# Optimization experiments

Hardware: AMD Instinct MI355X
Metric: run time of the kernel (lower is better)

The kernel has to match this reference:

```python
import jax, jax.numpy as jnp
import numpy as np

N, E, M, C = 4000, 60000, 16, 64        # nodes, edges, (lmax+1)^2, sphere_channels
H, HEADS, A, VC, CE, Z = 64, 8, 8, 8, 32, 90  # attn hidden, heads, alpha ch, value ch, edge ch, max elements


def _params(key):
    ks = jax.random.split(key, 10)
    g = lambda k, sh, fan: jax.random.normal(k, sh, dtype=jnp.float32) / np.float32(np.sqrt(fan))
    return [g(ks[0], (Z, CE), CE),          # emb_s: source atom embedding
            g(ks[1], (Z, CE), CE),          # emb_t: target atom embedding
            g(ks[2], (CE,), 1.0),           # w_d : distance projection
            g(ks[3], (CE, H), CE),          # We  : edge scalar -> hidden (m=0 inject)
            g(ks[4], (C, H), C),            # Ws  : source channel mix
            g(ks[5], (C, H), C),            # Wt  : target channel mix
            g(ks[6], (H, HEADS * A), H),    # Wa  : alpha features
            g(ks[7], (HEADS, A), A),        # va  : per-head alpha vector
            g(ks[8], (H, HEADS * VC), H),   # Wv  : values
            g(ks[9], (HEADS * VC, 1), HEADS * VC)]  # Wo : output proj (1 channel)


def setup_inputs() -> dict:
    key = jax.random.key(0)
    ks = jax.random.split(key, 8)
    x = jax.random.normal(ks[0], (N, M, C), dtype=jnp.float32)
    atomic_numbers = jax.random.randint(ks[1], (N,), 0, Z)
    edge_distance = jax.random.uniform(ks[2], (E,), dtype=jnp.float32) * 5.0 + 0.5
    edge_index = jax.random.randint(ks[3], (2, E), 0, N)
    noise_mask = jax.random.randint(ks[4], (N,), 0, 2).astype(bool)
    # per-edge SO3/Wigner rotation: random orthogonal [E, M, M]
    rng = np.random.default_rng(0)
    q, _ = np.linalg.qr(rng.standard_normal((E, M, M)).astype(np.float32))
    wigner = jnp.asarray(q, dtype=jnp.float32)
    names = ['emb_s', 'emb_t', 'w_d', 'We', 'Ws', 'Wt', 'Wa', 'va', 'Wv', 'Wo']
    inp = {'x': x, 'atomic_numbers': atomic_numbers, 'edge_distance': edge_distance,
           'edge_index': edge_index, 'noise_mask': noise_mask, 'wigner': wigner}
    for n, v in zip(names, _params(ks[5])):
        inp['fs_' + n] = v
    for n, v in zip(names, _params(ks[6])):
        inp['dn_' + n] = v
    return inp


def _block(x, zn, dist, src, dst, D, emb_s, emb_t, w_d, We, Ws, Wt, Wa, va, Wv, Wo):
    # gather + rotate edge-wise node features into edge-aligned frame
    xs = jnp.einsum('emn,enc->emc', D, x[src])            # [E,M,C]
    xt = jnp.einsum('emn,enc->emc', D, x[dst])            # [E,M,C]
    # scalar edge embedding (distance + source/target atom embeddings)
    e = jax.nn.silu(dist[:, None] * w_d + emb_s[zn[src]] + emb_t[zn[dst]])  # [E,CE]
    # SO2-style channel mixing; inject edge scalars into the m=0 (invariant) row
    f = jnp.einsum('emc,ch->emh', xs, Ws) + jnp.einsum('emc,ch->emh', xt, Wt)  # [E,M,H]
    f = f.at[:, 0, :].add(e @ We)
    # attention logits from the invariant part
    a = jax.nn.leaky_relu(f[:, 0, :] @ Wa, 0.2).reshape(E, HEADS, A)
    logits = jnp.einsum('eha,ha->eh', a, va)              # [E,HEADS]
    # segment softmax over incoming edges per target node
    mx = jax.ops.segment_max(logits, dst, num_segments=N)
    ex = jnp.exp(logits - mx[dst])
    alpha = ex / (jax.ops.segment_sum(ex, dst, num_segments=N)[dst] + 1e-9)
    # values, attention-weight, rotate back (D^T), scatter to nodes
    v = (f @ Wv).reshape(E, M, HEADS, VC) * alpha[:, None, :, None]
    v = jnp.einsum('emn,emhv->enhv', D, v).reshape(E, M, HEADS * VC)
    out = jax.ops.segment_sum(v, dst, num_segments=N) @ Wo  # [N,M,1]
    return out[:, 1:4, 0]  # narrow(1, 1, 3) -> l=1 vector components [N,3]


def reference(x, atomic_numbers, edge_distance, edge_index, noise_mask, wigner,
              fs_emb_s, fs_emb_t, fs_w_d, fs_We, fs_Ws, fs_Wt, fs_Wa, fs_va, fs_Wv, fs_Wo,
              dn_emb_s, dn_emb_t, dn_w_d, dn_We, dn_Ws, dn_Wt, dn_Wa, dn_va, dn_Wv, dn_Wo):
    src, dst = edge_index[0], edge_index[1]
    forces = _block(x, atomic_numbers, edge_distance, src, dst, wigner,
                    fs_emb_s, fs_emb_t, fs_w_d, fs_We, fs_Ws, fs_Wt, fs_Wa, fs_va, fs_Wv, fs_Wo)
    den = _block(x, atomic_numbers, edge_distance, src, dst, wigner,
                 dn_emb_s, dn_emb_t, dn_w_d, dn_We, dn_Ws, dn_Wt, dn_Wa, dn_va, dn_Wv, dn_Wo)
    # denoising_pos_forward with noise_mask: forces = den*mask + forces*~mask
    m = noise_mask[:, None].astype(x.dtype)
    return den * m + forces * (1.0 - m)
```

## Files before the change

kernel.cpp:

```cpp
#include <hip/hip_runtime.h>

typedef unsigned short ushort_t;
typedef __attribute__((ext_vector_type(8))) short short8;
typedef __attribute__((ext_vector_type(4))) float floatx4;

constexpr int RS = 11520;

__device__ inline float bf2f(ushort_t u) {
    union { unsigned int i; float f; } v; v.i = ((unsigned int)u) << 16; return v.f;
}
__device__ inline ushort_t f2bf(float f) {
    union { float f; unsigned int i; } v; v.f = f;
    unsigned int b = v.i + 0x7FFFu + ((v.i >> 16) & 1u);
    return (ushort_t)(b >> 16);
}

__global__ __launch_bounds__(256) void k_composites(
    const float* __restrict__ Ws0, const float* __restrict__ Wt0, const float* __restrict__ We0,
    const float* __restrict__ Wa0, const float* __restrict__ Wv0, const float* __restrict__ Wo0,
    const float* __restrict__ Ws1, const float* __restrict__ Wt1, const float* __restrict__ We1,
    const float* __restrict__ Wa1, const float* __restrict__ Wv1, const float* __restrict__ Wo1,
    float* __restrict__ cmp)
{
    int task = blockIdx.x;
    int r    = blockIdx.y;
    const float* Ws = r ? Ws1 : Ws0;
    const float* Wt = r ? Wt1 : Wt0;
    const float* We = r ? We1 : We0;
    const float* Wa = r ? Wa1 : Wa0;
    const float* Wv = r ? Wv1 : Wv0;
    const float* Wo = r ? Wo1 : Wo0;
    float* base = cmp + r * RS;

    if (task == 0 || task == 1) {
        const float* L = task ? Wt : Ws;
        float* out = base + task * 4096;
        for (int idx = threadIdx.x; idx < 4096; idx += 256) {
            int c = idx >> 6, j = idx & 63;
            float a = 0.f;
            for (int k = 0; k < 64; ++k) a += L[c * 64 + k] * Wa[k * 64 + j];
            out[idx] = a;
        }
    } else if (task == 2) {
        float* out = base + 8192;
        for (int idx = threadIdx.x; idx < 2048; idx += 256) {
            int ce = idx >> 6, j = idx & 63;
            float a = 0.f;
            for (int k = 0; k < 64; ++k) a += We[ce * 64 + k] * Wa[k * 64 + j];
            out[idx] = a;
        }
    } else {
        const float* L = (task == 3) ? Ws : (task == 4) ? Wt : We;
        int rows = (task == 5) ? 32 : 64;
        float* out = base + ((task == 3) ? 10240 : (task == 4) ? 10752 : 11264);
        for (int idx = threadIdx.x; idx < rows * 8; idx += 256) {
            int c = idx >> 3, h = idx & 7;
            float a = 0.f;
            for (int k = 0; k < 64; ++k) {
                float wv = 0.f;
                #pragma unroll
                for (int aa = 0; aa < 8; ++aa) wv += Wv[k * 64 + h * 8 + aa] * Wo[h * 8 + aa];
                a += L[c * 64 + k] * wv;
            }
            out[idx] = a;
        }
    }
}

__device__ inline short8 bfragW(const float* __restrict__ W, int colBase, int kBase,
                                int q, int n) {
    short8 f;
    #pragma unroll
    for (int j = 0; j < 8; ++j)
        f[j] = (short)f2bf(W[(kBase + q * 8 + j) * 64 + colBase + n]);
    return f;
}
__device__ inline short8 bfragP(const float* __restrict__ P0, const float* __restrict__ P1,
                                int kBase, int q, int n) {
    const float* P = (n < 8) ? P0 : P1;
    int c = n & 7;
    short8 f;
    #pragma unroll
    for (int j = 0; j < 8; ++j)
        f[j] = (short)f2bf(P[(kBase + q * 8 + j) * 8 + c]);
    return f;
}

#define MFMA(a, b, c) __builtin_amdgcn_mfma_f32_16x16x32_bf16((a), (b), (c), 0, 0, 0)

__global__ __launch_bounds__(256, 2) void k_node(
    const float* __restrict__ x, const int* __restrict__ mask,
    const float* __restrict__ cmp,
    float* __restrict__ psrc, float* __restrict__ ptgt,
    ushort_t* __restrict__ srcA, ushort_t* __restrict__ tgtA,
    int N, int totWaves)
{
    int wid  = (int)((blockIdx.x * blockDim.x + threadIdx.x) >> 6);
    int lane = threadIdx.x & 63;
    int q    = lane >> 4;
    int n16  = lane & 15;

    short8 Bs0[4][2], Bs1[4][2], Bt0[4][2], Bt1[4][2];
    #pragma unroll
    for (int t = 0; t < 4; ++t) {
        #pragma unroll
        for (int kh = 0; kh < 2; ++kh) {
            Bs0[t][kh] = bfragW(cmp,             t * 16, kh * 32, q, n16);
            Bs1[t][kh] = bfragW(cmp + RS,        t * 16, kh * 32, q, n16);
            Bt0[t][kh] = bfragW(cmp + 4096,      t * 16, kh * 32, q, n16);
            Bt1[t][kh] = bfragW(cmp + RS + 4096, t * 16, kh * 32, q, n16);
        }
    }
    short8 Bp[2], Bq[2];
    #pragma unroll
    for (int kh = 0; kh < 2; ++kh) {
        Bp[kh] = bfragP(cmp + 10240, cmp + RS + 10240, kh * 32, q, n16);
        Bq[kh] = bfragP(cmp + 10752, cmp + RS + 10752, kh * 32, q, n16);
    }

    const floatx4 zero = {0.f, 0.f, 0.f, 0.f};

    for (int nd = wid; nd < N; nd += totWaves) {
        const float* xp = x + (size_t)nd * 1024 + n16 * 64 + q * 8;
        float4 v0 = *(const float4*)(xp);
        float4 v1 = *(const float4*)(xp + 4);
        float4 v2 = *(const float4*)(xp + 32);
        float4 v3 = *(const float4*)(xp + 36);
        short8 a0, a1;
        a0[0] = (short)f2bf(v0.x); a0[1] = (short)f2bf(v0.y);
        a0[2] = (short)f2bf(v0.z); a0[3] = (short)f2bf(v0.w);
        a0[4] = (short)f2bf(v1.x); a0[5] = (short)f2bf(v1.y);
        a0[6] = (short)f2bf(v1.z); a0[7] = (short)f2bf(v1.w);
        a1[0] = (short)f2bf(v2.x); a1[1] = (short)f2bf(v2.y);
        a1[2] = (short)f2bf(v2.z); a1[3] = (short)f2bf(v2.w);
        a1[4] = (short)f2bf(v3.x); a1[5] = (short)f2bf(v3.y);
        a1[6] = (short)f2bf(v3.z); a1[7] = (short)f2bf(v3.w);

        int rsel = (mask[nd] != 0);

        {
            floatx4 c0 = zero, c1 = zero, c2 = zero, c3 = zero;
            c0 = MFMA(a0, Bs0[0][0], c0); c0 = MFMA(a1, Bs0[0][1], c0);
            c1 = MFMA(a0, Bs0[1][0], c1); c1 = MFMA(a1, Bs0[1][1], c1);
            c2 = MFMA(a0, Bs0[2][0], c2); c2 = MFMA(a1, Bs0[2][1], c2);
            c3 = MFMA(a0, Bs0[3][0], c3); c3 = MFMA(a1, Bs0[3][1], c3);
            ushort_t* sp = srcA + (size_t)nd * 2048 + (q * 4) * 64 + n16;
            #pragma unroll
            for (int rr = 0; rr < 4; ++rr) {
                sp[rr * 64 +  0] = f2bf(c0[rr]);
                sp[rr * 64 + 16] = f2bf(c1[rr]);
                sp[rr * 64 + 32] = f2bf(c2[rr]);
                sp[rr * 64 + 48] = f2bf(c3[rr]);
            }
        }
        {
            floatx4 c0 = zero, c1 = zero, c2 = zero, c3 = zero;
            c0 = MFMA(a0, Bs1[0][0], c0); c0 = MFMA(a1, Bs1[0][1], c0);
            c1 = MFMA(a0, Bs1[1][0], c1); c1 = MFMA(a1, Bs1[1][1], c1);
            c2 = MFMA(a0, Bs1[2][0], c2); c2 = MFMA(a1, Bs1[2][1], c2);
            c3 = MFMA(a0, Bs1[3][0], c3); c3 = MFMA(a1, Bs1[3][1], c3);
            ushort_t* sp = srcA + (size_t)nd * 2048 + 1024 + (q * 4) * 64 + n16;
            #pragma unroll
            for (int rr = 0; rr < 4; ++rr) {
                sp[rr * 64 +  0] = f2bf(c0[rr]);
                sp[rr * 64 + 16] = f2bf(c1[rr]);
                sp[rr * 64 + 32] = f2bf(c2[rr]);
                sp[rr * 64 + 48] = f2bf(c3[rr]);
            }
        }

        {
            floatx4 c0 = zero, c1 = zero, c2 = zero, c3 = zero;
            if (rsel) {
                c0 = MFMA(a0, Bt1[0][0], c0); c0 = MFMA(a1, Bt1[0][1], c0);
                c1 = MFMA(a0, Bt1[1][0], c1); c1 = MFMA(a1, Bt1[1][1], c1);
                c2 = MFMA(a0, Bt1[2][0], c2); c2 = MFMA(a1, Bt1[2][1], c2);
                c3 = MFMA(a0, Bt1[3][0], c3); c3 = MFMA(a1, Bt1[3][1], c3);
            } else {
                c0 = MFMA(a0, Bt0[0][0], c0); c0 = MFMA(a1, Bt0[0][1], c0);
                c1 = MFMA(a0, Bt0[1][0], c1); c1 = MFMA(a1, Bt0[1][1], c1);
                c2 = MFMA(a0, Bt0[2][0], c2); c2 = MFMA(a1, Bt0[2][1], c2);
                c3 = MFMA(a0, Bt0[3][0], c3); c3 = MFMA(a1, Bt0[3][1], c3);
            }
            ushort_t* tp = tgtA + (size_t)nd * 1024 + (q * 4) * 64 + n16;
            #pragma unroll
            for (int rr = 0; rr < 4; ++rr) {
                tp[rr * 64 +  0] = f2bf(c0[rr]);
                tp[rr * 64 + 16] = f2bf(c1[rr]);
                tp[rr * 64 + 32] = f2bf(c2[rr]);
                tp[rr * 64 + 48] = f2bf(c3[rr]);
            }
        }

        {
            floatx4 cp = zero;
            cp = MFMA(a0, Bp[0], cp); cp = MFMA(a1, Bp[1], cp);
            if (q == 0) {
                int r = n16 >> 3, h = n16 & 7;
                float* pp = psrc + (size_t)nd * 48 + r * 24 + h;
                pp[0]  = cp[1];
                pp[8]  = cp[2];
                pp[16] = cp[3];
            }
            floatx4 cq = zero;
            cq = MFMA(a0, Bq[0], cq); cq = MFMA(a1, Bq[1], cq);
            if (q == 0 && (n16 >> 3) == rsel) {
                int h = n16 & 7;
                float* pp = ptgt + (size_t)nd * 24 + h;
                pp[0]  = cq[1];
                pp[8]  = cq[2];
                pp[16] = cq[3];
            }
        }
    }
}

__global__ __launch_bounds__(256) void k_logits(
    const int* __restrict__ ei, const float* __restrict__ dist,
    const int* __restrict__ zn, const int* __restrict__ mask,
    const float* __restrict__ wig, const float* __restrict__ cmp,
    const float* __restrict__ embs0, const float* __restrict__ embt0, const float* __restrict__ wd0,
    const float* __restrict__ embs1, const float* __restrict__ embt1, const float* __restrict__ wd1,
    const float* __restrict__ va0, const float* __restrict__ va1,
    const ushort_t* __restrict__ srcA, const ushort_t* __restrict__ tgtA,
    float* __restrict__ den, float* __restrict__ exb, float* __restrict__ ejb, int E)
{
    int wv = threadIdx.x >> 6, j = threadIdx.x & 63;
    int e = blockIdx.x * 4 + wv;
    if (e >= E) return;
    int src = ei[e], dst = ei[E + e];
    int r = (mask[dst] != 0);
    float d = dist[e];
    int zs = zn[src], zt = zn[dst];

    float es;
    {
        int ce = j & 31;
        float z = r ? (d * wd1[ce] + embs1[zs * 32 + ce] + embt1[zt * 32 + ce])
                    : (d * wd0[ce] + embs0[zs * 32 + ce] + embt0[zt * 32 + ce]);
        es = z / (1.f + __expf(-z));
    }

    const float* WeWa   = cmp + r * RS + 8192;
    const float* WeWvWo = cmp + r * RS + 11264;
    int h8 = j & 7;
    float f0a = 0.f, ej = 0.f;
    #pragma unroll
    for (int ce = 0; ce < 32; ++ce) {
        float ev = __shfl(es, ce, 64);
        f0a += ev * WeWa[ce * 64 + j];
        ej  += ev * WeWvWo[ce * 8 + h8];
    }

    const ushort_t* sp = srcA + (size_t)src * 2048 + r * 1024 + j;
    const ushort_t* tp = tgtA + (size_t)dst * 1024 + j;
    const float* w0 = wig + (size_t)e * 256;
    #pragma unroll
    for (int n = 0; n < 16; ++n) {
        float sv = bf2f(sp[n * 64]) + bf2f(tp[n * 64]);
        f0a += w0[n] * sv;
    }

    float la = f0a > 0.f ? f0a : 0.2f * f0a;
    float val = la * (r ? va1[j] : va0[j]);
    val += __shfl_xor(val, 1);
    val += __shfl_xor(val, 2);
    val += __shfl_xor(val, 4);
    float ex = __expf(val);
    if (h8 == 0) {
        atomicAdd(&den[dst * 8 + (j >> 3)], ex);
        exb[(size_t)e * 8 + (j >> 3)] = ex;
    }
    if (j < 8) ejb[(size_t)e * 8 + j] = ej;
}

__global__ __launch_bounds__(256) void k_scatter(
    const int* __restrict__ ei, const int* __restrict__ mask,
    const float* __restrict__ wig,
    const float* __restrict__ psrc, const float* __restrict__ ptgt,
    const float* __restrict__ exb, const float* __restrict__ ejb,
    const float* __restrict__ den, float* __restrict__ out, int E)
{
    int t = threadIdx.x;
    int g = t >> 3, h = t & 7;
    int e = blockIdx.x * 32 + g;
    if (e >= E) return;
    int src = ei[e], dst = ei[E + e];
    int r = (mask[dst] != 0);
    float alpha = exb[(size_t)e * 8 + h] / (den[dst * 8 + h] + 1e-9f);
    const float* ps = psrc + (size_t)src * 48 + r * 24;
    const float* pt = ptgt + (size_t)dst * 24;
    float s0 = alpha * (ps[h]      + pt[h]);
    float s1 = alpha * (ps[8 + h]  + pt[8 + h]);
    float s2 = alpha * (ps[16 + h] + pt[16 + h]);
    float se = alpha * ejb[(size_t)e * 8 + h];
    #pragma unroll
    for (int off = 1; off < 8; off <<= 1) {
        s0 += __shfl_xor(s0, off);
        s1 += __shfl_xor(s1, off);
        s2 += __shfl_xor(s2, off);
        se += __shfl_xor(se, off);
    }
    if (h == 0) {
        const float* w0 = wig + (size_t)e * 256;
        atomicAdd(&out[dst * 3 + 0], s0 + w0[1] * se);
        atomicAdd(&out[dst * 3 + 1], s1 + w0[2] * se);
        atomicAdd(&out[dst * 3 + 2], s2 + w0[3] * se);
    }
}

extern "C" void kernel_launch(void* const* d_in, const int* in_sizes, int n_in,
                              void* d_out, int out_size, void* d_ws, size_t ws_size,
                              hipStream_t stream) {
    const float* x    = (const float*)d_in[0];
    const int*   zn   = (const int*)d_in[1];
    const float* dist = (const float*)d_in[2];
    const int*   ei   = (const int*)d_in[3];
    const int*   mask = (const int*)d_in[4];
    const float* wig  = (const float*)d_in[5];
    const float* fs[10]; const float* dn[10];
    for (int i = 0; i < 10; ++i) { fs[i] = (const float*)d_in[6 + i]; dn[i] = (const float*)d_in[16 + i]; }

    int N = in_sizes[1];
    int E = in_sizes[2];

    float* cmp  = (float*)d_ws;
    float* den  = cmp + 2 * RS;
    float* exb  = den + (size_t)N * 8;
    float* ejb  = exb + (size_t)E * 8;
    float* psrc = ejb + (size_t)E * 8;
    float* ptgt = psrc + (size_t)N * 48;
    ushort_t* srcA = (ushort_t*)(ptgt + (size_t)N * 24);
    ushort_t* tgtA = srcA + (size_t)N * 2048;

    hipMemsetAsync(d_out, 0, (size_t)out_size * sizeof(float), stream);
    hipMemsetAsync(den, 0, (size_t)N * 8 * sizeof(float), stream);

    k_composites<<<dim3(6, 2), 256, 0, stream>>>(
        fs[4], fs[5], fs[3], fs[6], fs[8], fs[9],
        dn[4], dn[5], dn[3], dn[6], dn[8], dn[9], cmp);

    int nodeBlocks = 512;
    int totWaves = nodeBlocks * (256 / 64);
    k_node<<<nodeBlocks, 256, 0, stream>>>(x, mask, cmp, psrc, ptgt, srcA, tgtA, N, totWaves);

    k_logits<<<(E + 3) / 4, 256, 0, stream>>>(
        ei, dist, zn, mask, wig, cmp,
        fs[0], fs[1], fs[2], dn[0], dn[1], dn[2],
        fs[7], dn[7], srcA, tgtA, den, exb, ejb, E);

    k_scatter<<<(E + 31) / 32, 256, 0, stream>>>(
        ei, mask, wig, psrc, ptgt, exb, ejb, den, (float*)d_out, E);
}
```

Before: 259.0 us.

## Fuse logits and scatter via per-node numerator accumulation, transpose node feature layout

Softmax normalisation is deferred: the logits kernel now atomically accumulates exp-weighted per-head numerators per destination node alongside the denominator. A small per-node kernel then divides and sums over heads, which removes the separate edge scatter kernel and the per-edge exb/ejb buffers. The srcA/tgtA layout is transposed so each lane writes packed 4-element bf16 stores and the edge kernel reads 16 contiguous values with vector loads. The node kernel grid also grows from 512 to 1000 blocks. The cost is more atomics per edge (24 numerator slots plus 8 denominator slots) in exchange for one fewer edge pass.

```diff
diff --git a/kernel.cpp b/kernel.cpp
--- a/kernel.cpp
+++ b/kernel.cpp
@@ -85,6 +85,12 @@
         f[j] = (short)f2bf(P[(kBase + q * 8 + j) * 8 + c]);
     return f;
 }
+__device__ inline void st4(ushort_t* dst, const floatx4& c) {
+    uint2 v;
+    v.x = (unsigned int)f2bf(c[0]) | ((unsigned int)f2bf(c[1]) << 16);
+    v.y = (unsigned int)f2bf(c[2]) | ((unsigned int)f2bf(c[3]) << 16);
+    *(uint2*)dst = v;
+}
 
 #define MFMA(a, b, c) __builtin_amdgcn_mfma_f32_16x16x32_bf16((a), (b), (c), 0, 0, 0)
 
@@ -144,14 +150,8 @@
             c1 = MFMA(a0, Bs0[1][0], c1); c1 = MFMA(a1, Bs0[1][1], c1);
             c2 = MFMA(a0, Bs0[2][0], c2); c2 = MFMA(a1, Bs0[2][1], c2);
             c3 = MFMA(a0, Bs0[3][0], c3); c3 = MFMA(a1, Bs0[3][1], c3);
-            ushort_t* sp = srcA + (size_t)nd * 2048 + (q * 4) * 64 + n16;
-            #pragma unroll
-            for (int rr = 0; rr < 4; ++rr) {
-                sp[rr * 64 +  0] = f2bf(c0[rr]);
-                sp[rr * 64 + 16] = f2bf(c1[rr]);
-                sp[rr * 64 + 32] = f2bf(c2[rr]);
-                sp[rr * 64 + 48] = f2bf(c3[rr]);
-            }
+            ushort_t* sp = srcA + (size_t)nd * 2048 + n16 * 16 + q * 4;
+            st4(sp, c0); st4(sp + 256, c1); st4(sp + 512, c2); st4(sp + 768, c3);
         }
         {
             floatx4 c0 = zero, c1 = zero, c2 = zero, c3 = zero;
@@ -159,14 +159,8 @@
             c1 = MFMA(a0, Bs1[1][0], c1); c1 = MFMA(a1, Bs1[1][1], c1);
             c2 = MFMA(a0, Bs1[2][0], c2); c2 = MFMA(a1, Bs1[2][1], c2);
             c3 = MFMA(a0, Bs1[3][0], c3); c3 = MFMA(a1, Bs1[3][1], c3);
-            ushort_t* sp = srcA + (size_t)nd * 2048 + 1024 + (q * 4) * 64 + n16;
-            #pragma unroll
-            for (int rr = 0; rr < 4; ++rr) {
-                sp[rr * 64 +  0] = f2bf(c0[rr]);
-                sp[rr * 64 + 16] = f2bf(c1[rr]);
-                sp[rr * 64 + 32] = f2bf(c2[rr]);
-                sp[rr * 64 + 48] = f2bf(c3[rr]);
-            }
+            ushort_t* sp = srcA + (size_t)nd * 2048 + 1024 + n16 * 16 + q * 4;
+            st4(sp, c0); st4(sp + 256, c1); st4(sp + 512, c2); st4(sp + 768, c3);
         }
 
         {
@@ -182,14 +176,8 @@
                 c2 = MFMA(a0, Bt0[2][0], c2); c2 = MFMA(a1, Bt0[2][1], c2);
                 c3 = MFMA(a0, Bt0[3][0], c3); c3 = MFMA(a1, Bt0[3][1], c3);
             }
-            ushort_t* tp = tgtA + (size_t)nd * 1024 + (q * 4) * 64 + n16;
-            #pragma unroll
-            for (int rr = 0; rr < 4; ++rr) {
-                tp[rr * 64 +  0] = f2bf(c0[rr]);
-                tp[rr * 64 + 16] = f2bf(c1[rr]);
-                tp[rr * 64 + 32] = f2bf(c2[rr]);
-                tp[rr * 64 + 48] = f2bf(c3[rr]);
-            }
+            ushort_t* tp = tgtA + (size_t)nd * 1024 + n16 * 16 + q * 4;
+            st4(tp, c0); st4(tp + 256, c1); st4(tp + 512, c2); st4(tp + 768, c3);
         }
 
         {
@@ -215,7 +203,7 @@
     }
 }
 
-__global__ __launch_bounds__(256) void k_logits(
+__global__ __launch_bounds__(256) void k_fused(
     const int* __restrict__ ei, const float* __restrict__ dist,
     const int* __restrict__ zn, const int* __restrict__ mask,
     const float* __restrict__ wig, const float* __restrict__ cmp,
@@ -223,7 +211,8 @@
     const float* __restrict__ embs1, const float* __restrict__ embt1, const float* __restrict__ wd1,
     const float* __restrict__ va0, const float* __restrict__ va1,
     const ushort_t* __restrict__ srcA, const ushort_t* __restrict__ tgtA,
-    float* __restrict__ den, float* __restrict__ exb, float* __restrict__ ejb, int E)
+    const float* __restrict__ psrc, const float* __restrict__ ptgt,
+    float* __restrict__ den, float* __restrict__ num, int E)
 {
     int wv = threadIdx.x >> 6, j = threadIdx.x & 63;
     int e = blockIdx.x * 4 + wv;
@@ -232,6 +221,23 @@
     int r = (mask[dst] != 0);
     float d = dist[e];
     int zs = zn[src], zt = zn[dst];
+    int hq = j >> 3, h8 = j & 7;
+
+    const float* w0 = wig + (size_t)e * 256;
+    float4 wA = *(const float4*)(w0);
+    float4 wB = *(const float4*)(w0 + 4);
+    float4 wC = *(const float4*)(w0 + 8);
+    float4 wD = *(const float4*)(w0 + 12);
+    const ushort_t* sa = srcA + (size_t)src * 2048 + r * 1024 + j * 16;
+    const ushort_t* ta = tgtA + (size_t)dst * 1024 + j * 16;
+    short8 sv0 = *(const short8*)(sa);
+    short8 sv1 = *(const short8*)(sa + 8);
+    short8 tv0 = *(const short8*)(ta);
+    short8 tv1 = *(const short8*)(ta + 8);
+    float pv = 0.f;
+    if (h8 < 3)
+        pv = psrc[(size_t)src * 48 + r * 24 + h8 * 8 + hq]
+           + ptgt[(size_t)dst * 24 + h8 * 8 + hq];
 
     float es;
     {
@@ -243,23 +249,30 @@
 
     const float* WeWa   = cmp + r * RS + 8192;
     const float* WeWvWo = cmp + r * RS + 11264;
-    int h8 = j & 7;
     float f0a = 0.f, ej = 0.f;
     #pragma unroll
     for (int ce = 0; ce < 32; ++ce) {
         float ev = __shfl(es, ce, 64);
         f0a += ev * WeWa[ce * 64 + j];
-        ej  += ev * WeWvWo[ce * 8 + h8];
-    }
-
-    const ushort_t* sp = srcA + (size_t)src * 2048 + r * 1024 + j;
-    const ushort_t* tp = tgtA + (size_t)dst * 1024 + j;
-    const float* w0 = wig + (size_t)e * 256;
-    #pragma unroll
-    for (int n = 0; n < 16; ++n) {
-        float sv = bf2f(sp[n * 64]) + bf2f(tp[n * 64]);
-        f0a += w0[n] * sv;
-    }
+        ej  += ev * WeWvWo[ce * 8 + hq];
+    }
+
+    f0a += wA.x * (bf2f((ushort_t)sv0[0]) + bf2f((ushort_t)tv0[0]));
+    f0a += wA.y * (bf2f((ushort_t)sv0[1]) + bf2f((ushort_t)tv0[1]));
+    f0a += wA.z * (bf2f((ushort_t)sv0[2]) + bf2f((ushort_t)tv0[2]));
+    f0a += wA.w * (bf2f((ushort_t)sv0[3]) + bf2f((ushort_t)tv0[3]));
+    f0a += wB.x * (bf2f((ushort_t)sv0[4]) + bf2f((ushort_t)tv0[4]));
+    f0a += wB.y * (bf2f((ushort_t)sv0[5]) + bf2f((ushort_t)tv0[5]));
+    f0a += wB.z * (bf2f((ushort_t)sv0[6]) + bf2f((ushort_t)tv0[6]));
+    f0a += wB.w * (bf2f((ushort_t)sv0[7]) + bf2f((ushort_t)tv0[7]));
+    f0a += wC.x * (bf2f((ushort_t)sv1[0]) + bf2f((ushort_t)tv1[0]));
+    f0a += wC.y * (bf2f((ushort_t)sv1[1]) + bf2f((ushort_t)tv1[1]));
+    f0a += wC.z * (bf2f((ushort_t)sv1[2]) + bf2f((ushort_t)tv1[2]));
+    f0a += wC.w * (bf2f((ushort_t)sv1[3]) + bf2f((ushort_t)tv1[3]));
+    f0a += wD.x * (bf2f((ushort_t)sv1[4]) + bf2f((ushort_t)tv1[4]));
+    f0a += wD.y * (bf2f((ushort_t)sv1[5]) + bf2f((ushort_t)tv1[5]));
+    f0a += wD.z * (bf2f((ushort_t)sv1[6]) + bf2f((ushort_t)tv1[6]));
+    f0a += wD.w * (bf2f((ushort_t)sv1[7]) + bf2f((ushort_t)tv1[7]));
 
     float la = f0a > 0.f ? f0a : 0.2f * f0a;
     float val = la * (r ? va1[j] : va0[j]);
@@ -267,46 +280,26 @@
     val += __shfl_xor(val, 2);
     val += __shfl_xor(val, 4);
     float ex = __expf(val);
-    if (h8 == 0) {
-        atomicAdd(&den[dst * 8 + (j >> 3)], ex);
-        exb[(size_t)e * 8 + (j >> 3)] = ex;
-    }
-    if (j < 8) ejb[(size_t)e * 8 + j] = ej;
-}
-
-__global__ __launch_bounds__(256) void k_scatter(
-    const int* __restrict__ ei, const int* __restrict__ mask,
-    const float* __restrict__ wig,
-    const float* __restrict__ psrc, const float* __restrict__ ptgt,
-    const float* __restrict__ exb, const float* __restrict__ ejb,
-    const float* __restrict__ den, float* __restrict__ out, int E)
+
+    if (h8 == 0) atomicAdd(&den[dst * 8 + hq], ex);
+    if (h8 < 3) {
+        float w0k = (h8 == 0) ? wA.y : (h8 == 1) ? wA.z : wA.w;
+        atomicAdd(&num[dst * 24 + hq * 3 + h8], ex * (pv + ej * w0k));
+    }
+}
+
+__global__ __launch_bounds__(256) void k_out(
+    const float* __restrict__ num, const float* __restrict__ den,
+    float* __restrict__ out, int N3)
 {
-    int t = threadIdx.x;
-    int g = t >> 3, h = t & 7;
-    int e = blockIdx.x * 32 + g;
-    if (e >= E) return;
-    int src = ei[e], dst = ei[E + e];
-    int r = (mask[dst] != 0);
-    float alpha = exb[(size_t)e * 8 + h] / (den[dst * 8 + h] + 1e-9f);
-    const float* ps = psrc + (size_t)src * 48 + r * 24;
-    const float* pt = ptgt + (size_t)dst * 24;
-    float s0 = alpha * (ps[h]      + pt[h]);
-    float s1 = alpha * (ps[8 + h]  + pt[8 + h]);
-    float s2 = alpha * (ps[16 + h] + pt[16 + h]);
-    float se = alpha * ejb[(size_t)e * 8 + h];
-    #pragma unroll
-    for (int off = 1; off < 8; off <<= 1) {
-        s0 += __shfl_xor(s0, off);
-        s1 += __shfl_xor(s1, off);
-        s2 += __shfl_xor(s2, off);
-        se += __shfl_xor(se, off);
-    }
-    if (h == 0) {
-        const float* w0 = wig + (size_t)e * 256;
-        atomicAdd(&out[dst * 3 + 0], s0 + w0[1] * se);
-        atomicAdd(&out[dst * 3 + 1], s1 + w0[2] * se);
-        atomicAdd(&out[dst * 3 + 2], s2 + w0[3] * se);
-    }
+    int t = blockIdx.x * 256 + threadIdx.x;
+    if (t >= N3) return;
+    int n = t / 3, k = t - n * 3;
+    float acc = 0.f;
+    #pragma unroll
+    for (int h = 0; h < 8; ++h)
+        acc += num[n * 24 + h * 3 + k] / (den[n * 8 + h] + 1e-9f);
+    out[t] = acc;
 }
 
 extern "C" void kernel_launch(void* const* d_in, const int* in_sizes, int n_in,
@@ -326,29 +319,27 @@
 
     float* cmp  = (float*)d_ws;
     float* den  = cmp + 2 * RS;
-    float* exb  = den + (size_t)N * 8;
-    float* ejb  = exb + (size_t)E * 8;
-    float* psrc = ejb + (size_t)E * 8;
+    float* num  = den + (size_t)N * 8;
+    float* psrc = num + (size_t)N * 24;
     float* ptgt = psrc + (size_t)N * 48;
     ushort_t* srcA = (ushort_t*)(ptgt + (size_t)N * 24);
     ushort_t* tgtA = srcA + (size_t)N * 2048;
 
     hipMemsetAsync(d_out, 0, (size_t)out_size * sizeof(float), stream);
-    hipMemsetAsync(den, 0, (size_t)N * 8 * sizeof(float), stream);
+    hipMemsetAsync(den, 0, (size_t)N * 32 * sizeof(float), stream);
 
     k_composites<<<dim3(6, 2), 256, 0, stream>>>(
         fs[4], fs[5], fs[3], fs[6], fs[8], fs[9],
         dn[4], dn[5], dn[3], dn[6], dn[8], dn[9], cmp);
 
-    int nodeBlocks = 512;
+    int nodeBlocks = 1000;
     int totWaves = nodeBlocks * (256 / 64);
     k_node<<<nodeBlocks, 256, 0, stream>>>(x, mask, cmp, psrc, ptgt, srcA, tgtA, N, totWaves);
 
-    k_logits<<<(E + 3) / 4, 256, 0, stream>>>(
+    k_fused<<<(E + 3) / 4, 256, 0, stream>>>(
         ei, dist, zn, mask, wig, cmp,
         fs[0], fs[1], fs[2], dn[0], dn[1], dn[2],
-        fs[7], dn[7], srcA, tgtA, den, exb, ejb, E);
-
-    k_scatter<<<(E + 31) / 32, 256, 0, stream>>>(
-        ei, mask, wig, psrc, ptgt, exb, ejb, den, (float*)d_out, E);
-}
+        fs[7], dn[7], srcA, tgtA, psrc, ptgt, den, num, E);
+
+    k_out<<<(N * 3 + 255) / 256, 256, 0, stream>>>(num, den, (float*)d_out, N * 3);
+}
```

Measured after the change: 244.1 us. -5.7%, faster.
